# Performance work log

Hardware: AMD Instinct MI355X
Metric: run time of the kernel (lower is better)

## Reference

```python
import jax, jax.numpy as jnp
import numpy as np

B, S, D, H, E = 8, 196, 768, 12, 8
HD = D // H  # 64
FF = 4 * D   # 3072
EPS = 1e-5


def setup_inputs() -> dict:
    key = jax.random.key(0)
    ks = jax.random.split(key, 12)
    s = 0.02
    inp = {
        'x': jax.random.normal(ks[0], (B, S, D), jnp.float32),
        'ln1_g': jnp.ones((D,), jnp.float32),
        'ln1_b': jnp.zeros((D,), jnp.float32),
        'Wq': jax.random.normal(ks[1], (D, D), jnp.float32) * s,
        'bq': jnp.zeros((D,), jnp.float32),
        'Wk': jax.random.normal(ks[2], (D, HD), jnp.float32) * s,
        'bk': jnp.zeros((HD,), jnp.float32),
        'Wv': jax.random.normal(ks[3], (D, HD), jnp.float32) * s,
        'bv': jnp.zeros((HD,), jnp.float32),
        'ln2_g': jnp.ones((D,), jnp.float32),
        'ln2_b': jnp.zeros((D,), jnp.float32),
        'Wg': jax.random.normal(ks[4], (D, E), jnp.float32) * s,
        'bg': jnp.zeros((E,), jnp.float32),
        'W1': jax.random.normal(ks[5], (E, D, FF), jnp.float32) * s,
        'b1': jnp.zeros((E, FF), jnp.float32),
        'W2': jax.random.normal(ks[6], (E, FF, D), jnp.float32) * s,
        'b2': jnp.zeros((E, D), jnp.float32),
    }
    return inp


def _layernorm(x, g, b):
    mu = jnp.mean(x, axis=-1, keepdims=True)
    var = jnp.var(x, axis=-1, keepdims=True)
    return (x - mu) * jax.lax.rsqrt(var + EPS) * g + b


def _rotate_half(x):
    x1, x2 = jnp.split(x, 2, axis=-1)
    return jnp.concatenate((-x2, x1), axis=-1)


def _rope(seq_len):
    inv_freq = 1.0 / (10000.0 ** (jnp.arange(0, HD, 2, dtype=jnp.float32) / HD))
    freqs = jnp.arange(seq_len, dtype=jnp.float32)[:, None] * inv_freq[None, :]
    emb = jnp.concatenate((freqs, freqs), axis=-1)  # [S, HD]
    return emb[None, :, None, :]  # [1, S, 1, HD]


def _attention(x, Wq, bq, Wk, bk, Wv, bv):
    b, s, _ = x.shape
    q = (x @ Wq + bq).reshape(b, s, H, HD)
    k = (x @ Wk + bk).reshape(b, s, 1, HD)
    v = (x @ Wv + bv).reshape(b, s, 1, HD)
    k = jnp.broadcast_to(k, (b, s, H, HD))
    v = jnp.broadcast_to(v, (b, s, H, HD))
    pe = _rope(s)
    cos, sin = jnp.cos(pe), jnp.sin(pe)
    q = q * cos + _rotate_half(q) * sin
    k = k * cos + _rotate_half(k) * sin
    scale = HD ** -0.5
    # NOTE: faithful to source -- matmul over the last two dims of [b,s,h,d],
    # i.e. attention across HEADS, not sequence positions.
    attn = jnp.einsum('bshd,bsgd->bshg', q, k) * scale
    attn = jax.nn.softmax(attn, axis=-1)
    out = jnp.einsum('bshg,bsgd->bshd', attn, v)
    return out.reshape(b, s, H * HD)


def _moe(x, Wg, bg, W1, b1, W2, b2):
    b, s, d = x.shape
    xt = x.reshape(-1, d)  # [T, D]
    gates = jax.nn.softmax(xt @ Wg + bg, axis=-1)
    top1 = jnp.argmax(gates, axis=-1)  # topk(k=2)[:,0] == argmax
    out = jnp.zeros_like(xt)
    for e in range(E):  # small fixed expert count
        h = jax.nn.gelu(xt @ W1[e] + b1[e], approximate=False)
        y = h @ W2[e] + b2[e]
        out = jnp.where((top1 == e)[:, None], y, out)
    return out.reshape(b, s, d)


def reference(x, ln1_g, ln1_b, Wq, bq, Wk, bk, Wv, bv, ln2_g, ln2_b, Wg, bg, W1, b1, W2, b2):
    res = x
    h = _layernorm(x, ln1_g, ln1_b)
    h = _attention(h, Wq, bq, Wk, bk, Wv, bv)
    x = res + h
    res = x
    h = _layernorm(x, ln2_g, ln2_b)
    h = _moe(h, Wg, bg, W1, b1, W2, b2)
    return res + h
```

## Files before the change

kernel.cpp:

```cpp
#include <hip/hip_runtime.h>
#include <hip/hip_bf16.h>


typedef unsigned short u16;
typedef short bf16x8_t __attribute__((ext_vector_type(8)));
typedef unsigned short u16x4_t __attribute__((ext_vector_type(4)));
typedef float f32x4_t  __attribute__((ext_vector_type(4)));

#define T_TOK 1568
#define DM 768
#define HD 64
#define FF 3072
#define NE 8

#define OFF_CNT   0
#define OFF_BUCK  256
#define OFF_H2    (OFF_BUCK + NE*T_TOK*4)
#define OFF_HMID  (OFF_H2 + T_TOK*DM*2)

__device__ __forceinline__ u16 f2bf(float f) {
    return __builtin_bit_cast(u16, __float2bfloat16(f));
}
__device__ __forceinline__ float gelu_f(float x) {
    return 0.5f * x * (1.0f + erff(x * 0.70710678118654752440f));
}

#define SFENCE() __builtin_amdgcn_sched_barrier(0)
#define RAW_BAR() __builtin_amdgcn_s_barrier()

__global__ __launch_bounds__(64) void k_front(
        const float* __restrict__ x,
        const float* __restrict__ g1, const float* __restrict__ b1,
        const float* __restrict__ Wv, const float* __restrict__ bv,
        const float* __restrict__ g2, const float* __restrict__ b2g,
        const float* __restrict__ Wg, const float* __restrict__ bg,
        const float* __restrict__ b2moe,
        u16* __restrict__ h2, float* __restrict__ out,
        int* __restrict__ cnt, int* __restrict__ buck) {
    __shared__ __align__(16) float h1s[DM];
    int t = blockIdx.x;
    int lane = threadIdx.x;

    const float* xp = x + (size_t)t * DM;
    f32x4_t xv[3];
    float s = 0.0f;
#pragma unroll
    for (int i = 0; i < 3; i++) {
        xv[i] = *(const f32x4_t*)&xp[4 * lane + 256 * i];
        s += xv[i][0] + xv[i][1] + xv[i][2] + xv[i][3];
    }
#pragma unroll
    for (int m = 1; m < 64; m <<= 1) s += __shfl_xor(s, m);
    float mu = s * (1.0f / DM);
    float vs = 0.0f;
#pragma unroll
    for (int i = 0; i < 3; i++)
#pragma unroll
        for (int m = 0; m < 4; m++) { float d = xv[i][m] - mu; vs += d * d; }
#pragma unroll
    for (int m = 1; m < 64; m <<= 1) vs += __shfl_xor(vs, m);
    float rs = rsqrtf(vs * (1.0f / DM) + 1e-5f);
#pragma unroll
    for (int i = 0; i < 3; i++) {
        int c = 4 * lane + 256 * i;
        f32x4_t gg = *(const f32x4_t*)&g1[c];
        f32x4_t bb = *(const f32x4_t*)&b1[c];
        f32x4_t h;
#pragma unroll
        for (int m = 0; m < 4; m++) h[m] = (xv[i][m] - mu) * rs * gg[m] + bb[m];
        *(f32x4_t*)&h1s[c] = h;
    }
    __syncthreads();

    int g = lane >> 4, sl = lane & 15;
    float a0 = 0.f, a1 = 0.f, a2 = 0.f, a3 = 0.f;
    {
        const float* wp = Wv + g * HD + 4 * sl;
#pragma unroll 8
        for (int kk = 0; kk < 192; kk++) {
            f32x4_t w4 = *(const f32x4_t*)&wp[(size_t)kk * (4 * HD)];
            float h = h1s[4 * kk + g];
            a0 += h * w4[0]; a1 += h * w4[1]; a2 += h * w4[2]; a3 += h * w4[3];
        }
    }
    a0 += __shfl_xor(a0, 16); a0 += __shfl_xor(a0, 32);
    a1 += __shfl_xor(a1, 16); a1 += __shfl_xor(a1, 32);
    a2 += __shfl_xor(a2, 16); a2 += __shfl_xor(a2, 32);
    a3 += __shfl_xor(a3, 16); a3 += __shfl_xor(a3, 32);
    f32x4_t bvv = *(const f32x4_t*)&bv[4 * sl];
    f32x4_t vv = { a0 + bvv[0], a1 + bvv[1], a2 + bvv[2], a3 + bvv[3] };

    float s2 = 0.0f;
#pragma unroll
    for (int i = 0; i < 3; i++)
#pragma unroll
        for (int m = 0; m < 4; m++) { xv[i][m] += vv[m]; s2 += xv[i][m]; }
#pragma unroll
    for (int m = 1; m < 64; m <<= 1) s2 += __shfl_xor(s2, m);
    float mu2 = s2 * (1.0f / DM);
    float vs2 = 0.0f;
#pragma unroll
    for (int i = 0; i < 3; i++)
#pragma unroll
        for (int m = 0; m < 4; m++) { float d = xv[i][m] - mu2; vs2 += d * d; }
#pragma unroll
    for (int m = 1; m < 64; m <<= 1) vs2 += __shfl_xor(vs2, m);
    float rs2 = rsqrtf(vs2 * (1.0f / DM) + 1e-5f);

    float le[NE];
#pragma unroll
    for (int e = 0; e < NE; e++) le[e] = 0.0f;
    u16* h2p = h2 + (size_t)t * DM;
#pragma unroll
    for (int i = 0; i < 3; i++) {
        int c = 4 * lane + 256 * i;
        f32x4_t gg = *(const f32x4_t*)&g2[c];
        f32x4_t bb = *(const f32x4_t*)&b2g[c];
        float h[4];
        u16x4_t hb;
#pragma unroll
        for (int m = 0; m < 4; m++) {
            h[m] = (xv[i][m] - mu2) * rs2 * gg[m] + bb[m];
            hb[m] = f2bf(h[m]);
        }
        *(u16x4_t*)&h2p[c] = hb;
#pragma unroll
        for (int m = 0; m < 4; m++) {
            f32x4_t w0 = *(const f32x4_t*)&Wg[(size_t)(c + m) * NE];
            f32x4_t w1 = *(const f32x4_t*)&Wg[(size_t)(c + m) * NE + 4];
            le[0] += h[m] * w0[0]; le[1] += h[m] * w0[1];
            le[2] += h[m] * w0[2]; le[3] += h[m] * w0[3];
            le[4] += h[m] * w1[0]; le[5] += h[m] * w1[1];
            le[6] += h[m] * w1[2]; le[7] += h[m] * w1[3];
        }
    }
#pragma unroll
    for (int e = 0; e < NE; e++) {
#pragma unroll
        for (int m = 1; m < 64; m <<= 1) le[e] += __shfl_xor(le[e], m);
    }
    float best = le[0] + bg[0]; int be = 0;
#pragma unroll
    for (int e = 1; e < NE; e++) {
        float q = le[e] + bg[e];
        if (q > best) { best = q; be = e; }
    }
    if (lane == 0) {
        int pos = atomicAdd(&cnt[be], 1);
        buck[be * T_TOK + pos] = t;
    }
    float* op = out + (size_t)t * DM;
    const float* bp = b2moe + (size_t)be * DM;
#pragma unroll
    for (int i = 0; i < 3; i++) {
        int c = 4 * lane + 256 * i;
        f32x4_t bbv = *(const f32x4_t*)&bp[c];
        f32x4_t o;
#pragma unroll
        for (int m = 0; m < 4; m++) o[m] = xv[i][m] + bbv[m];
        *(f32x4_t*)&op[c] = o;
    }
}

__global__ __launch_bounds__(256, 3) void k_moe_gemm1(
        const u16* __restrict__ h2, const float* __restrict__ W1,
        const float* __restrict__ b1, const int* __restrict__ cnt,
        const int* __restrict__ buck, u16* __restrict__ hmid) {
    int nt = blockIdx.x, e = blockIdx.y, mt = blockIdx.z;
    int cnte = cnt[e];
    int m0 = mt * 128;
    if (m0 >= cnte) return;
    int n0 = nt * 64;
    const float* W1e = W1 + (size_t)e * DM * FF;
    __shared__ __align__(16) u16 As[128 * 72];
    __shared__ __align__(16) u16 Bs[64 * 72];
    int tid = threadIdx.x, lane = tid & 63, wid = tid >> 6;

    int arow = tid >> 3, ac = tid & 7;
    int atok[4];
#pragma unroll
    for (int j = 0; j < 4; j++) {
        int i = m0 + arow + 32 * j;
        if (i >= cnte) i = cnte - 1;
        atok[j] = buck[e * T_TOK + i];
    }
    int bn = tid & 63, bkg = tid >> 6;

    f32x4_t acc[2][4];
#pragma unroll
    for (int mi = 0; mi < 2; mi++)
#pragma unroll
        for (int ni = 0; ni < 4; ni++) acc[mi][ni] = (f32x4_t){0.f, 0.f, 0.f, 0.f};

    bf16x8_t aP[4], aQ[4];
    float bP[16], bQ[16];

#define G_LOAD(SA, SB, KT) { \
    int k0_ = (KT) * 64; \
    _Pragma("unroll") \
    for (int j = 0; j < 4; j++) \
        SA[j] = *(const bf16x8_t*)&h2[(size_t)atok[j] * DM + k0_ + ac * 8]; \
    const float* bp_ = W1e + (size_t)(k0_ + bkg * 16) * FF + n0 + bn; \
    _Pragma("unroll") \
    for (int kk = 0; kk < 16; kk++) SB[kk] = bp_[(size_t)kk * FF]; \
}
#define STORE_LDS(SA, SB) { \
    _Pragma("unroll") \
    for (int j = 0; j < 4; j++) \
        *(bf16x8_t*)&As[(arow + 32 * j) * 72 + ac * 8] = SA[j]; \
    bf16x8_t p0_, p1_; \
    _Pragma("unroll") \
    for (int kk = 0; kk < 8; kk++) { \
        p0_[kk] = (short)f2bf(SB[kk]); \
        p1_[kk] = (short)f2bf(SB[kk + 8]); \
    } \
    *(bf16x8_t*)&Bs[bn * 72 + bkg * 16] = p0_; \
    *(bf16x8_t*)&Bs[bn * 72 + bkg * 16 + 8] = p1_; \
}
#define MFMA_TILE() { \
    int lr_ = lane & 15, q_ = lane >> 4; \
    _Pragma("unroll") \
    for (int s = 0; s < 2; s++) { \
        bf16x8_t af[2], bfr[4]; \
        _Pragma("unroll") \
        for (int mi = 0; mi < 2; mi++) \
            af[mi] = *(const bf16x8_t*)&As[(wid * 32 + mi * 16 + lr_) * 72 + s * 32 + q_ * 8]; \
        _Pragma("unroll") \
        for (int ni = 0; ni < 4; ni++) \
            bfr[ni] = *(const bf16x8_t*)&Bs[(ni * 16 + lr_) * 72 + s * 32 + q_ * 8]; \
        _Pragma("unroll") \
        for (int mi = 0; mi < 2; mi++) \
            _Pragma("unroll") \
            for (int ni = 0; ni < 4; ni++) \
                acc[mi][ni] = __builtin_amdgcn_mfma_f32_16x16x32_bf16( \
                    af[mi], bfr[ni], acc[mi][ni], 0, 0, 0); \
    } \
}
#define PHASE(SA, SB, PKT) { \
    SFENCE(); RAW_BAR(); SFENCE(); \
    STORE_LDS(SA, SB) \
    asm volatile("s_waitcnt lgkmcnt(0)" ::: "memory"); \
    SFENCE(); RAW_BAR(); SFENCE(); \
    if ((PKT) < 12) G_LOAD(SA, SB, PKT) \
    MFMA_TILE() \
}

    G_LOAD(aP, bP, 0)
    G_LOAD(aQ, bQ, 1)
    for (int kt = 0; kt < 12; kt += 2) {
        PHASE(aP, bP, kt + 2)
        PHASE(aQ, bQ, kt + 3)
    }
#undef G_LOAD
#undef STORE_LDS
#undef MFMA_TILE
#undef PHASE

    int lr = lane & 15, q = lane >> 4;
    float bias[4];
#pragma unroll
    for (int ni = 0; ni < 4; ni++) bias[ni] = b1[(size_t)e * FF + n0 + ni * 16 + lr];
#pragma unroll
    for (int mi = 0; mi < 2; mi++) {
#pragma unroll
        for (int r = 0; r < 4; r++) {
            int i = m0 + wid * 32 + mi * 16 + q * 4 + r;
            if (i < cnte) {
                int t = buck[e * T_TOK + i];
                size_t base = (size_t)t * FF + n0;
#pragma unroll
                for (int ni = 0; ni < 4; ni++) {
                    float vv = acc[mi][ni][r] + bias[ni];
                    hmid[base + ni * 16 + lr] = f2bf(gelu_f(vv));
                }
            }
        }
    }
}

__global__ __launch_bounds__(256, 3) void k_moe_gemm2(
        const u16* __restrict__ hmid, const float* __restrict__ W2,
        const int* __restrict__ cnt, const int* __restrict__ buck,
        float* __restrict__ out) {
    int nt = blockIdx.x, e = blockIdx.y, z = blockIdx.z;
    int kc = z & 3, mt = z >> 2;
    int cnte = cnt[e];
    int m0 = mt * 128;
    if (m0 >= cnte) return;
    int n0 = nt * 64;
    int kbase = kc * (FF / 4);
    const float* W2e = W2 + (size_t)e * FF * DM;
    __shared__ __align__(16) u16 As[128 * 72];
    __shared__ __align__(16) u16 Bs[64 * 72];
    int tid = threadIdx.x, lane = tid & 63, wid = tid >> 6;

    int arow = tid >> 3, ac = tid & 7;
    int atok[4];
#pragma unroll
    for (int j = 0; j < 4; j++) {
        int i = m0 + arow + 32 * j;
        if (i >= cnte) i = cnte - 1;
        atok[j] = buck[e * T_TOK + i];
    }
    int bn = tid & 63, bkg = tid >> 6;

    f32x4_t acc[2][4];
#pragma unroll
    for (int mi = 0; mi < 2; mi++)
#pragma unroll
        for (int ni = 0; ni < 4; ni++) acc[mi][ni] = (f32x4_t){0.f, 0.f, 0.f, 0.f};

    bf16x8_t aP[4], aQ[4];
    float bP[16], bQ[16];

#define G_LOAD(SA, SB, KT) { \
    int k0_ = kbase + (KT) * 64; \
    _Pragma("unroll") \
    for (int j = 0; j < 4; j++) \
        SA[j] = *(const bf16x8_t*)&hmid[(size_t)atok[j] * FF + k0_ + ac * 8]; \
    const float* bp_ = W2e + (size_t)(k0_ + bkg * 16) * DM + n0 + bn; \
    _Pragma("unroll") \
    for (int kk = 0; kk < 16; kk++) SB[kk] = bp_[(size_t)kk * DM]; \
}
#define STORE_LDS(SA, SB) { \
    _Pragma("unroll") \
    for (int j = 0; j < 4; j++) \
        *(bf16x8_t*)&As[(arow + 32 * j) * 72 + ac * 8] = SA[j]; \
    bf16x8_t p0_, p1_; \
    _Pragma("unroll") \
    for (int kk = 0; kk < 8; kk++) { \
        p0_[kk] = (short)f2bf(SB[kk]); \
        p1_[kk] = (short)f2bf(SB[kk + 8]); \
    } \
    *(bf16x8_t*)&Bs[bn * 72 + bkg * 16] = p0_; \
    *(bf16x8_t*)&Bs[bn * 72 + bkg * 16 + 8] = p1_; \
}
#define MFMA_TILE() { \
    int lr_ = lane & 15, q_ = lane >> 4; \
    _Pragma("unroll") \
    for (int s = 0; s < 2; s++) { \
        bf16x8_t af[2], bfr[4]; \
        _Pragma("unroll") \
        for (int mi = 0; mi < 2; mi++) \
            af[mi] = *(const bf16x8_t*)&As[(wid * 32 + mi * 16 + lr_) * 72 + s * 32 + q_ * 8]; \
        _Pragma("unroll") \
        for (int ni = 0; ni < 4; ni++) \
            bfr[ni] = *(const bf16x8_t*)&Bs[(ni * 16 + lr_) * 72 + s * 32 + q_ * 8]; \
        _Pragma("unroll") \
        for (int mi = 0; mi < 2; mi++) \
            _Pragma("unroll") \
            for (int ni = 0; ni < 4; ni++) \
                acc[mi][ni] = __builtin_amdgcn_mfma_f32_16x16x32_bf16( \
                    af[mi], bfr[ni], acc[mi][ni], 0, 0, 0); \
    } \
}
#define PHASE(SA, SB, PKT) { \
    SFENCE(); RAW_BAR(); SFENCE(); \
    STORE_LDS(SA, SB) \
    asm volatile("s_waitcnt lgkmcnt(0)" ::: "memory"); \
    SFENCE(); RAW_BAR(); SFENCE(); \
    if ((PKT) < 12) G_LOAD(SA, SB, PKT) \
    MFMA_TILE() \
}

    G_LOAD(aP, bP, 0)
    G_LOAD(aQ, bQ, 1)
    for (int kt = 0; kt < 12; kt += 2) {
        PHASE(aP, bP, kt + 2)
        PHASE(aQ, bQ, kt + 3)
    }
#undef G_LOAD
#undef STORE_LDS
#undef MFMA_TILE
#undef PHASE

    int lr = lane & 15, q = lane >> 4;
#pragma unroll
    for (int mi = 0; mi < 2; mi++) {
#pragma unroll
        for (int r = 0; r < 4; r++) {
            int i = m0 + wid * 32 + mi * 16 + q * 4 + r;
            if (i < cnte) {
                int t = buck[e * T_TOK + i];
                size_t base = (size_t)t * DM + n0;
#pragma unroll
                for (int ni = 0; ni < 4; ni++)
                    atomicAdd(&out[base + ni * 16 + lr], acc[mi][ni][r]);
            }
        }
    }
}

extern "C" void kernel_launch(void* const* d_in, const int* in_sizes, int n_in,
                              void* d_out, int out_size, void* d_ws, size_t ws_size,
                              hipStream_t stream) {
    const float* x    = (const float*)d_in[0];
    const float* ln1g = (const float*)d_in[1];
    const float* ln1b = (const float*)d_in[2];
    const float* Wv   = (const float*)d_in[7];
    const float* bv   = (const float*)d_in[8];
    const float* ln2g = (const float*)d_in[9];
    const float* ln2b = (const float*)d_in[10];
    const float* Wg   = (const float*)d_in[11];
    const float* bg   = (const float*)d_in[12];
    const float* W1   = (const float*)d_in[13];
    const float* b1   = (const float*)d_in[14];
    const float* W2   = (const float*)d_in[15];
    const float* b2   = (const float*)d_in[16];

    char* ws = (char*)d_ws;
    int*   cnt  = (int*)(ws + OFF_CNT);
    int*   buck = (int*)(ws + OFF_BUCK);
    u16*   h2   = (u16*)(ws + OFF_H2);
    u16*   hmid = (u16*)(ws + OFF_HMID);
    float* out  = (float*)d_out;

    hipMemsetAsync(cnt, 0, NE * sizeof(int), stream);
    k_front<<<T_TOK, 64, 0, stream>>>(x, ln1g, ln1b, Wv, bv, ln2g, ln2b,
                                      Wg, bg, b2, h2, out, cnt, buck);
    k_moe_gemm1<<<dim3(FF / 64, NE, 13), 256, 0, stream>>>(h2, W1, b1, cnt, buck, hmid);
    k_moe_gemm2<<<dim3(DM / 64, NE, 52), 256, 0, stream>>>(hmid, W2, cnt, buck, out);
}
```

Baseline: 276.6 us.

## Split front kernel into LN1/V-proj MFMA/gate and shrink MoE GEMM M-tiles

The fused per-token front kernel is split into three kernels: LayerNorm1 writing bf16, a batched V projection on MFMA using a hi/lo bf16 split of Wv to keep near-fp32 accuracy, and a gate/LN2 kernel. The per-token scalar GEMV that reread Wv for every token is meant to become a tiled matrix multiply. Both MoE GEMMs drop from 128-row to 64-row M tiles, load A fragments straight from global memory into registers instead of staging them in LDS, and raise the occupancy hint, giving more blocks per expert. The costs are two extra kernel launches, fp32 V stored to and reloaded from workspace, and more W1/W2 traffic because each weight tile is now reused across fewer tokens.

```diff
diff --git a/kernel.cpp b/kernel.cpp
--- a/kernel.cpp
+++ b/kernel.cpp
@@ -15,12 +15,18 @@
 
 #define OFF_CNT   0
 #define OFF_BUCK  256
-#define OFF_H2    (OFF_BUCK + NE*T_TOK*4)
+#define OFF_V     (OFF_BUCK + NE*T_TOK*4)
+#define OFF_H1    (OFF_V + T_TOK*HD*4)
+#define OFF_H2    (OFF_H1 + T_TOK*DM*2)
 #define OFF_HMID  (OFF_H2 + T_TOK*DM*2)
 
 __device__ __forceinline__ u16 f2bf(float f) {
     return __builtin_bit_cast(u16, __float2bfloat16(f));
 }
+__device__ __forceinline__ float bf2f(u16 h) {
+    unsigned u = ((unsigned)h) << 16;
+    return __builtin_bit_cast(float, u);
+}
 __device__ __forceinline__ float gelu_f(float x) {
     return 0.5f * x * (1.0f + erff(x * 0.70710678118654752440f));
 }
@@ -28,73 +34,158 @@
 #define SFENCE() __builtin_amdgcn_sched_barrier(0)
 #define RAW_BAR() __builtin_amdgcn_s_barrier()
 
-__global__ __launch_bounds__(64) void k_front(
-        const float* __restrict__ x,
-        const float* __restrict__ g1, const float* __restrict__ b1,
-        const float* __restrict__ Wv, const float* __restrict__ bv,
+__global__ __launch_bounds__(64) void k_ln1(const float* __restrict__ x,
+                                            const float* __restrict__ g1,
+                                            const float* __restrict__ b1,
+                                            u16* __restrict__ h1) {
+    int t = blockIdx.x, lane = threadIdx.x;
+    const float* xp = x + (size_t)t * DM;
+    f32x4_t xv[3];
+    float s = 0.0f;
+#pragma unroll
+    for (int i = 0; i < 3; i++) {
+        xv[i] = *(const f32x4_t*)&xp[4 * lane + 256 * i];
+        s += xv[i][0] + xv[i][1] + xv[i][2] + xv[i][3];
+    }
+#pragma unroll
+    for (int m = 1; m < 64; m <<= 1) s += __shfl_xor(s, m);
+    float mu = s * (1.0f / DM);
+    float vs = 0.0f;
+#pragma unroll
+    for (int i = 0; i < 3; i++)
+#pragma unroll
+        for (int m = 0; m < 4; m++) { float d = xv[i][m] - mu; vs += d * d; }
+#pragma unroll
+    for (int m = 1; m < 64; m <<= 1) vs += __shfl_xor(vs, m);
+    float rs = rsqrtf(vs * (1.0f / DM) + 1e-5f);
+    u16* hp = h1 + (size_t)t * DM;
+#pragma unroll
+    for (int i = 0; i < 3; i++) {
+        int c = 4 * lane + 256 * i;
+        f32x4_t gg = *(const f32x4_t*)&g1[c];
+        f32x4_t bb = *(const f32x4_t*)&b1[c];
+        u16x4_t hb;
+#pragma unroll
+        for (int m = 0; m < 4; m++) hb[m] = f2bf((xv[i][m] - mu) * rs * gg[m] + bb[m]);
+        *(u16x4_t*)&hp[c] = hb;
+    }
+}
+
+__global__ __launch_bounds__(256) void k_vproj(
+        const u16* __restrict__ h1, const float* __restrict__ Wv,
+        const float* __restrict__ bv, float* __restrict__ vws) {
+    __shared__ __align__(16) u16 Bh[64 * 72];
+    __shared__ __align__(16) u16 Bl[64 * 72];
+    int m0 = blockIdx.x * 64;
+    int tid = threadIdx.x, lane = tid & 63, wid = tid >> 6;
+    int bn = tid & 63, bkg = tid >> 6;
+    int lr = lane & 15, q = lane >> 4;
+    int row = m0 + wid * 16 + lr;
+    if (row >= T_TOK) row = T_TOK - 1;
+    const u16* ap = h1 + (size_t)row * DM;
+
+    f32x4_t acc[4];
+#pragma unroll
+    for (int ni = 0; ni < 4; ni++) acc[ni] = (f32x4_t){0.f, 0.f, 0.f, 0.f};
+
+    bf16x8_t aP[2], aQ[2];
+    float bP[16], bQ[16];
+
+#define G_LOAD_A(SA, KT) { \
+    int k0_ = (KT) * 64; \
+    SA[0] = *(const bf16x8_t*)&ap[k0_ + q * 8]; \
+    SA[1] = *(const bf16x8_t*)&ap[k0_ + 32 + q * 8]; \
+}
+#define G_LOAD_B(SB, KT) { \
+    const float* bp_ = Wv + (size_t)((KT) * 64 + bkg * 16) * HD + bn; \
+    _Pragma("unroll") \
+    for (int kk = 0; kk < 16; kk++) SB[kk] = bp_[(size_t)kk * HD]; \
+}
+#define STORE_B(SB) { \
+    bf16x8_t h0_, h1_, l0_, l1_; \
+    _Pragma("unroll") \
+    for (int kk = 0; kk < 8; kk++) { \
+        float w0 = SB[kk], w1 = SB[kk + 8]; \
+        u16 hh0 = f2bf(w0), hh1 = f2bf(w1); \
+        h0_[kk] = (short)hh0; h1_[kk] = (short)hh1; \
+        l0_[kk] = (short)f2bf(w0 - bf2f(hh0)); \
+        l1_[kk] = (short)f2bf(w1 - bf2f(hh1)); \
+    } \
+    *(bf16x8_t*)&Bh[bn * 72 + bkg * 16] = h0_; \
+    *(bf16x8_t*)&Bh[bn * 72 + bkg * 16 + 8] = h1_; \
+    *(bf16x8_t*)&Bl[bn * 72 + bkg * 16] = l0_; \
+    *(bf16x8_t*)&Bl[bn * 72 + bkg * 16 + 8] = l1_; \
+}
+#define MFMA_TILE(SA) { \
+    _Pragma("unroll") \
+    for (int s = 0; s < 2; s++) { \
+        bf16x8_t bh_[4], bl_[4]; \
+        _Pragma("unroll") \
+        for (int ni = 0; ni < 4; ni++) { \
+            bh_[ni] = *(const bf16x8_t*)&Bh[(ni * 16 + lr) * 72 + s * 32 + q * 8]; \
+            bl_[ni] = *(const bf16x8_t*)&Bl[(ni * 16 + lr) * 72 + s * 32 + q * 8]; \
+        } \
+        _Pragma("unroll") \
+        for (int ni = 0; ni < 4; ni++) { \
+            acc[ni] = __builtin_amdgcn_mfma_f32_16x16x32_bf16( \
+                SA[s], bh_[ni], acc[ni], 0, 0, 0); \
+            acc[ni] = __builtin_amdgcn_mfma_f32_16x16x32_bf16( \
+                SA[s], bl_[ni], acc[ni], 0, 0, 0); \
+        } \
+    } \
+}
+#define PHASE(SA, SB, PKT) { \
+    SFENCE(); RAW_BAR(); SFENCE(); \
+    STORE_B(SB) \
+    asm volatile("s_waitcnt lgkmcnt(0)" ::: "memory"); \
+    SFENCE(); RAW_BAR(); SFENCE(); \
+    if ((PKT) < 12) G_LOAD_B(SB, PKT) \
+    MFMA_TILE(SA) \
+    if ((PKT) < 12) G_LOAD_A(SA, PKT) \
+}
+
+    G_LOAD_A(aP, 0) G_LOAD_B(bP, 0)
+    G_LOAD_A(aQ, 1) G_LOAD_B(bQ, 1)
+    for (int kt = 0; kt < 12; kt += 2) {
+        PHASE(aP, bP, kt + 2)
+        PHASE(aQ, bQ, kt + 3)
+    }
+#undef G_LOAD_A
+#undef G_LOAD_B
+#undef STORE_B
+#undef MFMA_TILE
+#undef PHASE
+
+#pragma unroll
+    for (int ni = 0; ni < 4; ni++) {
+        float bb = bv[ni * 16 + lr];
+#pragma unroll
+        for (int r = 0; r < 4; r++) {
+            int i = m0 + wid * 16 + q * 4 + r;
+            if (i < T_TOK) vws[(size_t)i * HD + ni * 16 + lr] = acc[ni][r] + bb;
+        }
+    }
+}
+
+__global__ __launch_bounds__(64) void k_gate(
+        const float* __restrict__ x, const float* __restrict__ vws,
         const float* __restrict__ g2, const float* __restrict__ b2g,
         const float* __restrict__ Wg, const float* __restrict__ bg,
         const float* __restrict__ b2moe,
         u16* __restrict__ h2, float* __restrict__ out,
         int* __restrict__ cnt, int* __restrict__ buck) {
-    __shared__ __align__(16) float h1s[DM];
-    int t = blockIdx.x;
-    int lane = threadIdx.x;
-
+    int t = blockIdx.x, lane = threadIdx.x;
+    int sl = lane & 15;
     const float* xp = x + (size_t)t * DM;
     f32x4_t xv[3];
-    float s = 0.0f;
+    f32x4_t vv = *(const f32x4_t*)&vws[(size_t)t * HD + 4 * sl];
+    float s2 = 0.0f;
 #pragma unroll
     for (int i = 0; i < 3; i++) {
         xv[i] = *(const f32x4_t*)&xp[4 * lane + 256 * i];
-        s += xv[i][0] + xv[i][1] + xv[i][2] + xv[i][3];
-    }
-#pragma unroll
-    for (int m = 1; m < 64; m <<= 1) s += __shfl_xor(s, m);
-    float mu = s * (1.0f / DM);
-    float vs = 0.0f;
-#pragma unroll
-    for (int i = 0; i < 3; i++)
-#pragma unroll
-        for (int m = 0; m < 4; m++) { float d = xv[i][m] - mu; vs += d * d; }
-#pragma unroll
-    for (int m = 1; m < 64; m <<= 1) vs += __shfl_xor(vs, m);
-    float rs = rsqrtf(vs * (1.0f / DM) + 1e-5f);
-#pragma unroll
-    for (int i = 0; i < 3; i++) {
-        int c = 4 * lane + 256 * i;
-        f32x4_t gg = *(const f32x4_t*)&g1[c];
-        f32x4_t bb = *(const f32x4_t*)&b1[c];
-        f32x4_t h;
-#pragma unroll
-        for (int m = 0; m < 4; m++) h[m] = (xv[i][m] - mu) * rs * gg[m] + bb[m];
-        *(f32x4_t*)&h1s[c] = h;
-    }
-    __syncthreads();
-
-    int g = lane >> 4, sl = lane & 15;
-    float a0 = 0.f, a1 = 0.f, a2 = 0.f, a3 = 0.f;
-    {
-        const float* wp = Wv + g * HD + 4 * sl;
-#pragma unroll 8
-        for (int kk = 0; kk < 192; kk++) {
-            f32x4_t w4 = *(const f32x4_t*)&wp[(size_t)kk * (4 * HD)];
-            float h = h1s[4 * kk + g];
-            a0 += h * w4[0]; a1 += h * w4[1]; a2 += h * w4[2]; a3 += h * w4[3];
-        }
-    }
-    a0 += __shfl_xor(a0, 16); a0 += __shfl_xor(a0, 32);
-    a1 += __shfl_xor(a1, 16); a1 += __shfl_xor(a1, 32);
-    a2 += __shfl_xor(a2, 16); a2 += __shfl_xor(a2, 32);
-    a3 += __shfl_xor(a3, 16); a3 += __shfl_xor(a3, 32);
-    f32x4_t bvv = *(const f32x4_t*)&bv[4 * sl];
-    f32x4_t vv = { a0 + bvv[0], a1 + bvv[1], a2 + bvv[2], a3 + bvv[3] };
-
-    float s2 = 0.0f;
-#pragma unroll
-    for (int i = 0; i < 3; i++)
 #pragma unroll
         for (int m = 0; m < 4; m++) { xv[i][m] += vv[m]; s2 += xv[i][m]; }
+    }
 #pragma unroll
     for (int m = 1; m < 64; m <<= 1) s2 += __shfl_xor(s2, m);
     float mu2 = s2 * (1.0f / DM);
@@ -142,8 +233,8 @@
     float best = le[0] + bg[0]; int be = 0;
 #pragma unroll
     for (int e = 1; e < NE; e++) {
-        float q = le[e] + bg[e];
-        if (q > best) { best = q; be = e; }
+        float qv = le[e] + bg[e];
+        if (qv > best) { best = qv; be = e; }
     }
     if (lane == 0) {
         int pos = atomicAdd(&cnt[be], 1);
@@ -162,52 +253,43 @@
     }
 }
 
-__global__ __launch_bounds__(256, 3) void k_moe_gemm1(
+__global__ __launch_bounds__(256, 4) void k_moe_gemm1(
         const u16* __restrict__ h2, const float* __restrict__ W1,
         const float* __restrict__ b1, const int* __restrict__ cnt,
         const int* __restrict__ buck, u16* __restrict__ hmid) {
     int nt = blockIdx.x, e = blockIdx.y, mt = blockIdx.z;
     int cnte = cnt[e];
-    int m0 = mt * 128;
+    int m0 = mt * 64;
     if (m0 >= cnte) return;
     int n0 = nt * 64;
     const float* W1e = W1 + (size_t)e * DM * FF;
-    __shared__ __align__(16) u16 As[128 * 72];
     __shared__ __align__(16) u16 Bs[64 * 72];
     int tid = threadIdx.x, lane = tid & 63, wid = tid >> 6;
-
-    int arow = tid >> 3, ac = tid & 7;
-    int atok[4];
-#pragma unroll
-    for (int j = 0; j < 4; j++) {
-        int i = m0 + arow + 32 * j;
-        if (i >= cnte) i = cnte - 1;
-        atok[j] = buck[e * T_TOK + i];
-    }
     int bn = tid & 63, bkg = tid >> 6;
-
-    f32x4_t acc[2][4];
-#pragma unroll
-    for (int mi = 0; mi < 2; mi++)
-#pragma unroll
-        for (int ni = 0; ni < 4; ni++) acc[mi][ni] = (f32x4_t){0.f, 0.f, 0.f, 0.f};
-
-    bf16x8_t aP[4], aQ[4];
+    int lr = lane & 15, q = lane >> 4;
+
+    int arow = m0 + wid * 16 + lr;
+    if (arow >= cnte) arow = cnte - 1;
+    const u16* ap = h2 + (size_t)buck[e * T_TOK + arow] * DM;
+
+    f32x4_t acc[4];
+#pragma unroll
+    for (int ni = 0; ni < 4; ni++) acc[ni] = (f32x4_t){0.f, 0.f, 0.f, 0.f};
+
+    bf16x8_t aP[2], aQ[2];
     float bP[16], bQ[16];
 
-#define G_LOAD(SA, SB, KT) { \
+#define G_LOAD_A(SA, KT) { \
     int k0_ = (KT) * 64; \
-    _Pragma("unroll") \
-    for (int j = 0; j < 4; j++) \
-        SA[j] = *(const bf16x8_t*)&h2[(size_t)atok[j] * DM + k0_ + ac * 8]; \
-    const float* bp_ = W1e + (size_t)(k0_ + bkg * 16) * FF + n0 + bn; \
+    SA[0] = *(const bf16x8_t*)&ap[k0_ + q * 8]; \
+    SA[1] = *(const bf16x8_t*)&ap[k0_ + 32 + q * 8]; \
+}
+#define G_LOAD_B(SB, KT) { \
+    const float* bp_ = W1e + (size_t)((KT) * 64 + bkg * 16) * FF + n0 + bn; \
     _Pragma("unroll") \
     for (int kk = 0; kk < 16; kk++) SB[kk] = bp_[(size_t)kk * FF]; \
 }
-#define STORE_LDS(SA, SB) { \
-    _Pragma("unroll") \
-    for (int j = 0; j < 4; j++) \
-        *(bf16x8_t*)&As[(arow + 32 * j) * 72 + ac * 8] = SA[j]; \
+#define STORE_B(SB) { \
     bf16x8_t p0_, p1_; \
     _Pragma("unroll") \
     for (int kk = 0; kk < 8; kk++) { \
@@ -217,115 +299,96 @@
     *(bf16x8_t*)&Bs[bn * 72 + bkg * 16] = p0_; \
     *(bf16x8_t*)&Bs[bn * 72 + bkg * 16 + 8] = p1_; \
 }
-#define MFMA_TILE() { \
-    int lr_ = lane & 15, q_ = lane >> 4; \
+#define MFMA_TILE(SA) { \
     _Pragma("unroll") \
     for (int s = 0; s < 2; s++) { \
-        bf16x8_t af[2], bfr[4]; \
-        _Pragma("unroll") \
-        for (int mi = 0; mi < 2; mi++) \
-            af[mi] = *(const bf16x8_t*)&As[(wid * 32 + mi * 16 + lr_) * 72 + s * 32 + q_ * 8]; \
+        bf16x8_t bfr[4]; \
         _Pragma("unroll") \
         for (int ni = 0; ni < 4; ni++) \
-            bfr[ni] = *(const bf16x8_t*)&Bs[(ni * 16 + lr_) * 72 + s * 32 + q_ * 8]; \
-        _Pragma("unroll") \
-        for (int mi = 0; mi < 2; mi++) \
-            _Pragma("unroll") \
-            for (int ni = 0; ni < 4; ni++) \
-                acc[mi][ni] = __builtin_amdgcn_mfma_f32_16x16x32_bf16( \
-                    af[mi], bfr[ni], acc[mi][ni], 0, 0, 0); \
+            bfr[ni] = *(const bf16x8_t*)&Bs[(ni * 16 + lr) * 72 + s * 32 + q * 8]; \
+        _Pragma("unroll") \
+        for (int ni = 0; ni < 4; ni++) \
+            acc[ni] = __builtin_amdgcn_mfma_f32_16x16x32_bf16( \
+                SA[s], bfr[ni], acc[ni], 0, 0, 0); \
     } \
 }
 #define PHASE(SA, SB, PKT) { \
     SFENCE(); RAW_BAR(); SFENCE(); \
-    STORE_LDS(SA, SB) \
+    STORE_B(SB) \
     asm volatile("s_waitcnt lgkmcnt(0)" ::: "memory"); \
     SFENCE(); RAW_BAR(); SFENCE(); \
-    if ((PKT) < 12) G_LOAD(SA, SB, PKT) \
-    MFMA_TILE() \
-}
-
-    G_LOAD(aP, bP, 0)
-    G_LOAD(aQ, bQ, 1)
+    if ((PKT) < 12) G_LOAD_B(SB, PKT) \
+    MFMA_TILE(SA) \
+    if ((PKT) < 12) G_LOAD_A(SA, PKT) \
+}
+
+    G_LOAD_A(aP, 0) G_LOAD_B(bP, 0)
+    G_LOAD_A(aQ, 1) G_LOAD_B(bQ, 1)
     for (int kt = 0; kt < 12; kt += 2) {
         PHASE(aP, bP, kt + 2)
         PHASE(aQ, bQ, kt + 3)
     }
-#undef G_LOAD
-#undef STORE_LDS
+#undef G_LOAD_A
+#undef G_LOAD_B
+#undef STORE_B
 #undef MFMA_TILE
 #undef PHASE
 
-    int lr = lane & 15, q = lane >> 4;
     float bias[4];
 #pragma unroll
     for (int ni = 0; ni < 4; ni++) bias[ni] = b1[(size_t)e * FF + n0 + ni * 16 + lr];
 #pragma unroll
-    for (int mi = 0; mi < 2; mi++) {
-#pragma unroll
-        for (int r = 0; r < 4; r++) {
-            int i = m0 + wid * 32 + mi * 16 + q * 4 + r;
-            if (i < cnte) {
-                int t = buck[e * T_TOK + i];
-                size_t base = (size_t)t * FF + n0;
-#pragma unroll
-                for (int ni = 0; ni < 4; ni++) {
-                    float vv = acc[mi][ni][r] + bias[ni];
-                    hmid[base + ni * 16 + lr] = f2bf(gelu_f(vv));
-                }
-            }
+    for (int r = 0; r < 4; r++) {
+        int i = m0 + wid * 16 + q * 4 + r;
+        if (i < cnte) {
+            int t = buck[e * T_TOK + i];
+            size_t base = (size_t)t * FF + n0;
+#pragma unroll
+            for (int ni = 0; ni < 4; ni++)
+                hmid[base + ni * 16 + lr] = f2bf(gelu_f(acc[ni][r] + bias[ni]));
         }
     }
 }
 
-__global__ __launch_bounds__(256, 3) void k_moe_gemm2(
+__global__ __launch_bounds__(256, 4) void k_moe_gemm2(
         const u16* __restrict__ hmid, const float* __restrict__ W2,
         const int* __restrict__ cnt, const int* __restrict__ buck,
         float* __restrict__ out) {
     int nt = blockIdx.x, e = blockIdx.y, z = blockIdx.z;
     int kc = z & 3, mt = z >> 2;
     int cnte = cnt[e];
-    int m0 = mt * 128;
+    int m0 = mt * 64;
     if (m0 >= cnte) return;
     int n0 = nt * 64;
     int kbase = kc * (FF / 4);
     const float* W2e = W2 + (size_t)e * FF * DM;
-    __shared__ __align__(16) u16 As[128 * 72];
     __shared__ __align__(16) u16 Bs[64 * 72];
     int tid = threadIdx.x, lane = tid & 63, wid = tid >> 6;
-
-    int arow = tid >> 3, ac = tid & 7;
-    int atok[4];
-#pragma unroll
-    for (int j = 0; j < 4; j++) {
-        int i = m0 + arow + 32 * j;
-        if (i >= cnte) i = cnte - 1;
-        atok[j] = buck[e * T_TOK + i];
-    }
     int bn = tid & 63, bkg = tid >> 6;
-
-    f32x4_t acc[2][4];
-#pragma unroll
-    for (int mi = 0; mi < 2; mi++)
-#pragma unroll
-        for (int ni = 0; ni < 4; ni++) acc[mi][ni] = (f32x4_t){0.f, 0.f, 0.f, 0.f};
-
-    bf16x8_t aP[4], aQ[4];
+    int lr = lane & 15, q = lane >> 4;
+
+    int arow = m0 + wid * 16 + lr;
+    if (arow >= cnte) arow = cnte - 1;
+    const u16* ap = hmid + (size_t)buck[e * T_TOK + arow] * FF + kbase;
+
+    f32x4_t acc[4];
+#pragma unroll
+    for (int ni = 0; ni < 4; ni++) acc[ni] = (f32x4_t){0.f, 0.f, 0.f, 0.f};
+
+    bf16x8_t aP[2], aQ[2];
     float bP[16], bQ[16];
 
-#define G_LOAD(SA, SB, KT) { \
-    int k0_ = kbase + (KT) * 64; \
-    _Pragma("unroll") \
-    for (int j = 0; j < 4; j++) \
-        SA[j] = *(const bf16x8_t*)&hmid[(size_t)atok[j] * FF + k0_ + ac * 8]; \
-    const float* bp_ = W2e + (size_t)(k0_ + bkg * 16) * DM + n0 + bn; \
+#define G_LOAD_A(SA, KT) { \
+    int k0_ = (KT) * 64; \
+    SA[0] = *(const bf16x8_t*)&ap[k0_ + q * 8]; \
+    SA[1] = *(const bf16x8_t*)&ap[k0_ + 32 + q * 8]; \
+}
+#define G_LOAD_B(SB, KT) { \
+    const float* bp_ = W2e + (size_t)(kbase + (KT) * 64 + bkg * 16) * DM + n0 + bn; \
     _Pragma("unroll") \
     for (int kk = 0; kk < 16; kk++) SB[kk] = bp_[(size_t)kk * DM]; \
 }
-#define STORE_LDS(SA, SB) { \
-    _Pragma("unroll") \
-    for (int j = 0; j < 4; j++) \
-        *(bf16x8_t*)&As[(arow + 32 * j) * 72 + ac * 8] = SA[j]; \
+#define STORE_B(SB) { \
     bf16x8_t p0_, p1_; \
     _Pragma("unroll") \
     for (int kk = 0; kk < 8; kk++) { \
@@ -335,58 +398,50 @@
     *(bf16x8_t*)&Bs[bn * 72 + bkg * 16] = p0_; \
     *(bf16x8_t*)&Bs[bn * 72 + bkg * 16 + 8] = p1_; \
 }
-#define MFMA_TILE() { \
-    int lr_ = lane & 15, q_ = lane >> 4; \
+#define MFMA_TILE(SA) { \
     _Pragma("unroll") \
     for (int s = 0; s < 2; s++) { \
-        bf16x8_t af[2], bfr[4]; \
-        _Pragma("unroll") \
-        for (int mi = 0; mi < 2; mi++) \
-            af[mi] = *(const bf16x8_t*)&As[(wid * 32 + mi * 16 + lr_) * 72 + s * 32 + q_ * 8]; \
+        bf16x8_t bfr[4]; \
         _Pragma("unroll") \
         for (int ni = 0; ni < 4; ni++) \
-            bfr[ni] = *(const bf16x8_t*)&Bs[(ni * 16 + lr_) * 72 + s * 32 + q_ * 8]; \
-        _Pragma("unroll") \
-        for (int mi = 0; mi < 2; mi++) \
-            _Pragma("unroll") \
-            for (int ni = 0; ni < 4; ni++) \
-                acc[mi][ni] = __builtin_amdgcn_mfma_f32_16x16x32_bf16( \
-                    af[mi], bfr[ni], acc[mi][ni], 0, 0, 0); \
+            bfr[ni] = *(const bf16x8_t*)&Bs[(ni * 16 + lr) * 72 + s * 32 + q * 8]; \
+        _Pragma("unroll") \
+        for (int ni = 0; ni < 4; ni++) \
+            acc[ni] = __builtin_amdgcn_mfma_f32_16x16x32_bf16( \
+                SA[s], bfr[ni], acc[ni], 0, 0, 0); \
     } \
 }
 #define PHASE(SA, SB, PKT) { \
     SFENCE(); RAW_BAR(); SFENCE(); \
-    STORE_LDS(SA, SB) \
+    STORE_B(SB) \
     asm volatile("s_waitcnt lgkmcnt(0)" ::: "memory"); \
     SFENCE(); RAW_BAR(); SFENCE(); \
-    if ((PKT) < 12) G_LOAD(SA, SB, PKT) \
-    MFMA_TILE() \
-}
-
-    G_LOAD(aP, bP, 0)
-    G_LOAD(aQ, bQ, 1)
+    if ((PKT) < 12) G_LOAD_B(SB, PKT) \
+    MFMA_TILE(SA) \
+    if ((PKT) < 12) G_LOAD_A(SA, PKT) \
+}
+
+    G_LOAD_A(aP, 0) G_LOAD_B(bP, 0)
+    G_LOAD_A(aQ, 1) G_LOAD_B(bQ, 1)
     for (int kt = 0; kt < 12; kt += 2) {
         PHASE(aP, bP, kt + 2)
         PHASE(aQ, bQ, kt + 3)
     }
-#undef G_LOAD
-#undef STORE_LDS
+#undef G_LOAD_A
+#undef G_LOAD_B
+#undef STORE_B
 #undef MFMA_TILE
 #undef PHASE
 
-    int lr = lane & 15, q = lane >> 4;
-#pragma unroll
-    for (int mi = 0; mi < 2; mi++) {
-#pragma unroll
-        for (int r = 0; r < 4; r++) {
-            int i = m0 + wid * 32 + mi * 16 + q * 4 + r;
-            if (i < cnte) {
-                int t = buck[e * T_TOK + i];
-                size_t base = (size_t)t * DM + n0;
-#pragma unroll
-                for (int ni = 0; ni < 4; ni++)
-                    atomicAdd(&out[base + ni * 16 + lr], acc[mi][ni][r]);
-            }
+#pragma unroll
+    for (int r = 0; r < 4; r++) {
+        int i = m0 + wid * 16 + q * 4 + r;
+        if (i < cnte) {
+            int t = buck[e * T_TOK + i];
+            size_t base = (size_t)t * DM + n0;
+#pragma unroll
+            for (int ni = 0; ni < 4; ni++)
+                atomicAdd(&out[base + ni * 16 + lr], acc[ni][r]);
         }
     }
 }
@@ -411,13 +466,17 @@
     char* ws = (char*)d_ws;
     int*   cnt  = (int*)(ws + OFF_CNT);
     int*   buck = (int*)(ws + OFF_BUCK);
+    float* vws  = (float*)(ws + OFF_V);
+    u16*   h1   = (u16*)(ws + OFF_H1);
     u16*   h2   = (u16*)(ws + OFF_H2);
     u16*   hmid = (u16*)(ws + OFF_HMID);
     float* out  = (float*)d_out;
 
     hipMemsetAsync(cnt, 0, NE * sizeof(int), stream);
-    k_front<<<T_TOK, 64, 0, stream>>>(x, ln1g, ln1b, Wv, bv, ln2g, ln2b,
-                                      Wg, bg, b2, h2, out, cnt, buck);
-    k_moe_gemm1<<<dim3(FF / 64, NE, 13), 256, 0, stream>>>(h2, W1, b1, cnt, buck, hmid);
-    k_moe_gemm2<<<dim3(DM / 64, NE, 52), 256, 0, stream>>>(hmid, W2, cnt, buck, out);
-}
+    k_ln1<<<T_TOK, 64, 0, stream>>>(x, ln1g, ln1b, h1);
+    k_vproj<<<(T_TOK + 63) / 64, 256, 0, stream>>>(h1, Wv, bv, vws);
+    k_gate<<<T_TOK, 64, 0, stream>>>(x, vws, ln2g, ln2b, Wg, bg, b2,
+                                     h2, out, cnt, buck);
+    k_moe_gemm1<<<dim3(FF / 64, NE, 25), 256, 0, stream>>>(h2, W1, b1, cnt, buck, hmid);
+    k_moe_gemm2<<<dim3(DM / 64, NE, 100), 256, 0, stream>>>(hmid, W2, cnt, buck, out);
+}
```

Measured after the change: 295.3 us. +6.8%, slower.
